# Kernel tuning notes

Hardware: AMD Instinct MI355X
Metric: run time of the kernel (lower is better)

## Reference

```python
import jax, jax.numpy as jnp
import numpy as np

# ---- module config (init kwargs) ----
EMB = 256
HIDDEN = 256
L, H, P = 4, 8, 4
CH = HIDDEN // H
PADDING_MODE = "zeros"   # 'zeros' or 'border'
ALIGN_CORNERS = False
# feature pyramid level shapes (height, width), static
SHAPES = np.array([[128, 128], [64, 64], [32, 32], [16, 16]], dtype=np.int32)
LEVEL_STARTS = np.concatenate([[0], np.cumsum(SHAPES.prod(-1))[:-1]]).astype(np.int32)

B, N = 8, 1024
I = int(SHAPES.prod(-1).sum())  # 21760


def setup_inputs() -> dict:
    key = jax.random.key(0)
    ks = jax.random.split(key, 8)
    scale = 0.02
    return {
        "img": jax.random.normal(ks[0], (B, I, EMB), jnp.float32),
        "img_shapes": jnp.asarray(SHAPES),
        "queries": jax.random.normal(ks[1], (B, N, EMB), jnp.float32),
        "reference_points": jax.random.uniform(ks[2], (B, N, 2), dtype=jnp.float32),
        "W_img": jax.random.normal(ks[3], (EMB, HIDDEN), jnp.float32) * scale,
        "b_img": jnp.zeros((HIDDEN,), jnp.float32),
        "W_q": jax.random.normal(ks[4], (EMB, H * L * P * 3), jnp.float32) * scale,
        "b_q": jnp.zeros((H * L * P * 3,), jnp.float32),
        "W_out": jax.random.normal(ks[5], (HIDDEN, EMB), jnp.float32) * scale,
        "b_out": jnp.zeros((EMB,), jnp.float32),
    }


def _msda(img, points, attn):
    """Multiscale deformable attention core.
    img:    [B, I, H, CH] flattened pyramid features
    points: [B, N, H, L, P, 2] (x, y) in [0, 1]
    attn:   [B, N, H, L, P]
    returns [B, N, H, CH]
    """
    b, _, h_, ch = img.shape
    n = points.shape[1]
    img_t = img.transpose(0, 2, 1, 3)  # [B, H, I, CH]
    levels = []
    for l in range(L):
        hh, ww = int(SHAPES[l, 0]), int(SHAPES[l, 1])
        start = int(LEVEL_STARTS[l])
        p = points[:, :, :, l]  # [B, N, H, P, 2]
        # grid_sample pixel mapping (after the module's 2*p-1 normalization)
        if ALIGN_CORNERS:
            x = p[..., 0] * (ww - 1)
            y = p[..., 1] * (hh - 1)
        else:
            x = p[..., 0] * ww - 0.5
            y = p[..., 1] * hh - 0.5
        x0 = jnp.floor(x); y0 = jnp.floor(y)
        wx = x - x0;       wy = y - y0
        x0i = x0.astype(jnp.int32); y0i = y0.astype(jnp.int32)
        acc = jnp.zeros((b, h_, n * P, ch), img.dtype)
        corners = [
            (x0i,     y0i,     (1 - wx) * (1 - wy)),
            (x0i + 1, y0i,     wx * (1 - wy)),
            (x0i,     y0i + 1, (1 - wx) * wy),
            (x0i + 1, y0i + 1, wx * wy),
        ]
        for xi, yi, cw in corners:
            if PADDING_MODE == "zeros":
                valid = (xi >= 0) & (xi < ww) & (yi >= 0) & (yi < hh)
                cw = cw * valid.astype(cw.dtype)
            xc = jnp.clip(xi, 0, ww - 1)
            yc = jnp.clip(yi, 0, hh - 1)
            idx = start + yc * ww + xc                              # [B, N, H, P]
            idx_t = idx.transpose(0, 2, 1, 3).reshape(b, h_, n * P)  # [B, H, N*P]
            g = jnp.take_along_axis(img_t, idx_t[..., None], axis=2)  # [B, H, N*P, CH]
            cw_t = cw.transpose(0, 2, 1, 3).reshape(b, h_, n * P, 1)
            acc = acc + cw_t * g
        levels.append(acc.reshape(b, h_, n, P, ch))
    samples = jnp.stack(levels, axis=3)            # [B, H, N, L, P, CH]
    attn_t = attn.transpose(0, 2, 1, 3, 4)          # [B, H, N, L, P]
    return jnp.einsum("bhnlpc,bhnlp->bnhc", samples, attn_t)


def reference(img, img_shapes, queries, reference_points, W_img, b_img, W_q, b_q, W_out, b_out):
    b, i_, _ = img.shape
    n = queries.shape[1]
    qp = (queries @ W_q + b_q).reshape(b, n, H, L, P, 3)
    offsets = qp[..., :2]                            # [B, N, H, L, P, 2]
    attn = jax.nn.softmax(qp[..., 2].reshape(b, n, H, L * P), axis=-1).reshape(b, n, H, L, P)
    img_p = (img @ W_img + b_img).reshape(b, i_, H, CH)
    shapes_f = img_shapes.astype(jnp.float32)        # [L, 2] (h, w)
    # faithful to source: offsets / img_shapes[:, None, :]
    sampling_points = reference_points[:, :, None, None, None, :] + offsets / shapes_f[:, None, :]
    out = _msda(img_p, sampling_points, attn)        # [B, N, H, CH]
    return out.reshape(b, n, HIDDEN) @ W_out + b_out
```

## Files before the change

### kernel.cpp

```cpp
#include <hip/hip_runtime.h>
#include <type_traits>
#include <utility>

#define B_    8
#define NQ_   1024
#define I_    21760
#define EMB_  256
#define HID_  256
#define H_    8
#define CH_   32

typedef float  f32x4  __attribute__((ext_vector_type(4)));
typedef __bf16 bf16x8 __attribute__((ext_vector_type(8)));
typedef short  s16x8  __attribute__((ext_vector_type(8)));

template <typename V, typename = void>
struct bf16_mfma_native : std::false_type {};
template <typename V>
struct bf16_mfma_native<V, std::void_t<decltype(__builtin_amdgcn_mfma_f32_16x16x32_bf16(
    std::declval<V>(), std::declval<V>(), std::declval<f32x4>(), 0, 0, 0))>>
    : std::true_type {};

template <typename V>
__device__ __forceinline__ f32x4 mfma_dispatch(V a, V b, f32x4 c) {
  if constexpr (bf16_mfma_native<V>::value) {
    return __builtin_amdgcn_mfma_f32_16x16x32_bf16(a, b, c, 0, 0, 0);
  } else {
    return __builtin_amdgcn_mfma_f32_16x16x32_bf16(
        __builtin_bit_cast(s16x8, a), __builtin_bit_cast(s16x8, b), c, 0, 0, 0);
  }
}

__device__ __forceinline__ f32x4 MFMA(s16x8 a, s16x8 b, f32x4 c) {
  return mfma_dispatch(__builtin_bit_cast(bf16x8, a), __builtin_bit_cast(bf16x8, b), c);
}

__device__ __forceinline__ unsigned short f2bf(float f) {
  unsigned u = __float_as_uint(f);
  u += 0x7fffu + ((u >> 16) & 1u);
  return (unsigned short)(u >> 16);
}

template <int NS, bool OUT_BF16>
__global__ __launch_bounds__(512) void gemm_k256(
    const float* __restrict__ A, const float* __restrict__ W,
    const float* __restrict__ bias, void* __restrict__ Out,
    const int N, const int Mtiles) {
  __shared__ __align__(16) short lds[32 * 264];
  const int tid  = threadIdx.x;
  const int lane = tid & 63;
  const int wave = tid >> 6;
  const int quad = lane >> 4;
  const int ln   = lane & 15;

  s16x8 bfrag[NS][8];
  float bv[NS];
#pragma unroll
  for (int st = 0; st < NS; ++st) {
    const int ng = st * 128 + wave * 16 + ln;
    bv[st] = bias[ng];
#pragma unroll
    for (int ks = 0; ks < 8; ++ks) {
      s16x8 f;
#pragma unroll
      for (int j = 0; j < 8; ++j)
        f[j] = (short)f2bf(W[(ks * 32 + quad * 8 + j) * N + ng]);
      bfrag[st][ks] = f;
    }
  }

  const int sr = tid >> 4;
  const int sc = (tid & 15) * 16;

  for (int t = blockIdx.x; t < Mtiles; t += gridDim.x) {
    const size_t rowBase = (size_t)t * 32;
    {
      const float4* src = (const float4*)(A + (rowBase + sr) * 256 + sc);
      float4 v0 = src[0], v1 = src[1], v2 = src[2], v3 = src[3];
      s16x8 p0, p1;
      p0[0] = (short)f2bf(v0.x); p0[1] = (short)f2bf(v0.y);
      p0[2] = (short)f2bf(v0.z); p0[3] = (short)f2bf(v0.w);
      p0[4] = (short)f2bf(v1.x); p0[5] = (short)f2bf(v1.y);
      p0[6] = (short)f2bf(v1.z); p0[7] = (short)f2bf(v1.w);
      p1[0] = (short)f2bf(v2.x); p1[1] = (short)f2bf(v2.y);
      p1[2] = (short)f2bf(v2.z); p1[3] = (short)f2bf(v2.w);
      p1[4] = (short)f2bf(v3.x); p1[5] = (short)f2bf(v3.y);
      p1[6] = (short)f2bf(v3.z); p1[7] = (short)f2bf(v3.w);
      *(s16x8*)&lds[sr * 264 + sc]     = p0;
      *(s16x8*)&lds[sr * 264 + sc + 8] = p1;
    }
    __syncthreads();

    f32x4 acc[NS][2];
#pragma unroll
    for (int st = 0; st < NS; ++st) {
      acc[st][0] = f32x4{bv[st], bv[st], bv[st], bv[st]};
      acc[st][1] = acc[st][0];
    }
#pragma unroll
    for (int ks = 0; ks < 8; ++ks) {
      s16x8 a0 = *(const s16x8*)&lds[ln * 264 + ks * 32 + quad * 8];
      s16x8 a1 = *(const s16x8*)&lds[(ln + 16) * 264 + ks * 32 + quad * 8];
#pragma unroll
      for (int st = 0; st < NS; ++st) {
        acc[st][0] = MFMA(a0, bfrag[st][ks], acc[st][0]);
        acc[st][1] = MFMA(a1, bfrag[st][ks], acc[st][1]);
      }
    }
#pragma unroll
    for (int st = 0; st < NS; ++st) {
      const int ng = st * 128 + wave * 16 + ln;
#pragma unroll
      for (int rt = 0; rt < 2; ++rt) {
#pragma unroll
        for (int r = 0; r < 4; ++r) {
          const size_t m = rowBase + rt * 16 + quad * 4 + r;
          if constexpr (OUT_BF16)
            ((unsigned short*)Out)[m * N + ng] = f2bf(acc[st][rt][r]);
          else
            ((float*)Out)[m * N + ng] = acc[st][rt][r];
        }
      }
    }
    __syncthreads();
  }
}

__global__ __launch_bounds__(256) void softmax_points_kernel(
    const float* __restrict__ qp, const float* __restrict__ refp,
    float* __restrict__ attn, float* __restrict__ pts) {
  const int gid = blockIdx.x * 256 + threadIdx.x;
  const int q = gid >> 3, h = gid & 7;
  const float* base = qp + (size_t)q * 384 + h * 48;

  float s[16];
  float mx = -1e30f;
#pragma unroll
  for (int lp = 0; lp < 16; ++lp) {
    s[lp] = base[lp * 3 + 2];
    mx = fmaxf(mx, s[lp]);
  }
  float sum = 0.f;
#pragma unroll
  for (int lp = 0; lp < 16; ++lp) {
    s[lp] = __expf(s[lp] - mx);
    sum += s[lp];
  }
  const float inv = 1.0f / sum;
  float* ao = attn + (size_t)gid * 16;
#pragma unroll
  for (int lp = 0; lp < 16; ++lp) ao[lp] = s[lp] * inv;

  const float rx = refp[q * 2], ry = refp[q * 2 + 1];
  float* po = pts + (size_t)gid * 32;
  const float invsh[4] = {1.f / 128.f, 1.f / 64.f, 1.f / 32.f, 1.f / 16.f};
#pragma unroll
  for (int l = 0; l < 4; ++l) {
#pragma unroll
    for (int p = 0; p < 4; ++p) {
      const int lp = l * 4 + p;
      po[lp * 2 + 0] = rx + base[lp * 3 + 0] * invsh[l];
      po[lp * 2 + 1] = ry + base[lp * 3 + 1] * invsh[l];
    }
  }
}

__global__ __launch_bounds__(128) void msda_sample_kernel(
    const unsigned int* __restrict__ imgp,
    const float* __restrict__ attn, const float* __restrict__ pts,
    float* __restrict__ out) {
  __shared__ __align__(16) float sw[128][4];
  __shared__ __align__(16) int   sib[128][4];
  const int bid = blockIdx.x;
  const int b = bid >> 10;
  const int tid = threadIdx.x;

  {
    const int h = tid >> 4, lp = tid & 15, l = lp >> 2;
    const int dims[4]   = {128, 64, 32, 16};
    const int starts[4] = {0, 16384, 20480, 21504};
    const int ww = dims[l], hh = dims[l], start = starts[l];
    const float px = pts[((size_t)bid * 8 + h) * 32 + lp * 2 + 0];
    const float py = pts[((size_t)bid * 8 + h) * 32 + lp * 2 + 1];
    const float a  = attn[((size_t)bid * 8 + h) * 16 + lp];
    const float x = px * (float)ww - 0.5f;
    const float y = py * (float)hh - 0.5f;
    const float x0f = floorf(x), y0f = floorf(y);
    const float wx = x - x0f, wy = y - y0f;
    const int x0 = (int)x0f, y0 = (int)y0f;
    const float cw[4] = {(1.f - wx) * (1.f - wy), wx * (1.f - wy),
                         (1.f - wx) * wy,          wx * wy};
#pragma unroll
    for (int c = 0; c < 4; ++c) {
      const int xi = x0 + (c & 1), yi = y0 + (c >> 1);
      const bool valid = (xi >= 0) & (xi < ww) & (yi >= 0) & (yi < hh);
      const int xc = min(max(xi, 0), ww - 1);
      const int yc = min(max(yi, 0), hh - 1);
      const int idx = start + yc * ww + xc;
      sw[tid][c]  = valid ? a * cw[c] : 0.f;
      sib[tid][c] = ((b * I_ + idx) << 7) + (h << 4);
    }
  }
  __syncthreads();

  const int h = tid >> 4, c2 = tid & 15;
  float acc0 = 0.f, acc1 = 0.f;
#pragma unroll
  for (int lp = 0; lp < 16; ++lp) {
    const float4 w4 = *(const float4*)sw[h * 16 + lp];
    const int4   i4 = *(const int4*)sib[h * 16 + lp];
    unsigned u;
    u = imgp[i4.x + c2];
    acc0 += w4.x * __uint_as_float(u << 16);
    acc1 += w4.x * __uint_as_float(u & 0xffff0000u);
    u = imgp[i4.y + c2];
    acc0 += w4.y * __uint_as_float(u << 16);
    acc1 += w4.y * __uint_as_float(u & 0xffff0000u);
    u = imgp[i4.z + c2];
    acc0 += w4.z * __uint_as_float(u << 16);
    acc1 += w4.z * __uint_as_float(u & 0xffff0000u);
    u = imgp[i4.w + c2];
    acc0 += w4.w * __uint_as_float(u << 16);
    acc1 += w4.w * __uint_as_float(u & 0xffff0000u);
  }
  float2 r;
  r.x = acc0;
  r.y = acc1;
  *(float2*)&out[(size_t)bid * 256 + h * 32 + c2 * 2] = r;
}

#define OFF_IMGP 0ULL
#define OFF_QP   89128960ULL
#define OFF_ATTN 101711872ULL
#define OFF_PTS  105906176ULL
#define OFF_MSDA 114294784ULL
#define WS_NEEDED 122683392ULL

extern "C" void kernel_launch(void* const* d_in, const int* in_sizes, int n_in,
                              void* d_out, int out_size, void* d_ws, size_t ws_size,
                              hipStream_t stream) {
  const float* img     = (const float*)d_in[0];
  const float* queries = (const float*)d_in[2];
  const float* refp    = (const float*)d_in[3];
  const float* W_img   = (const float*)d_in[4];
  const float* b_img   = (const float*)d_in[5];
  const float* W_q     = (const float*)d_in[6];
  const float* b_q     = (const float*)d_in[7];
  const float* W_out   = (const float*)d_in[8];
  const float* b_out   = (const float*)d_in[9];

  if (ws_size < WS_NEEDED) return;

  char* ws = (char*)d_ws;
  unsigned short* imgp = (unsigned short*)(ws + OFF_IMGP);
  float* qp   = (float*)(ws + OFF_QP);
  float* attn = (float*)(ws + OFF_ATTN);
  float* pts  = (float*)(ws + OFF_PTS);
  float* msda = (float*)(ws + OFF_MSDA);

  hipLaunchKernelGGL((gemm_k256<2, true>), dim3(512), dim3(512), 0, stream,
                     img, W_img, b_img, (void*)imgp, 256, I_ * B_ / 32);
  hipLaunchKernelGGL((gemm_k256<3, false>), dim3(256), dim3(512), 0, stream,
                     queries, W_q, b_q, (void*)qp, 384, B_ * NQ_ / 32);
  hipLaunchKernelGGL(softmax_points_kernel, dim3(B_ * NQ_ * H_ / 256), dim3(256), 0, stream,
                     qp, refp, attn, pts);
  hipLaunchKernelGGL(msda_sample_kernel, dim3(B_ * NQ_), dim3(128), 0, stream,
                     (const unsigned int*)imgp, attn, pts, msda);
  hipLaunchKernelGGL((gemm_k256<2, false>), dim3(256), dim3(512), 0, stream,
                     msda, W_out, b_out, d_out, 256, B_ * NQ_ / 32);
}
```

Baseline: 337.8 us.

## Fuse query projection with softmax and widen MSDA sampling per thread

Merges the query projection GEMM and the softmax/sampling-point kernel into one kernel, so the 384-wide projection is staged in shared memory rather than written to and reread from global memory. This removes one launch and the qp buffer. The MSDA sampler now handles 4 queries per 256-thread block, and each thread loads 4 bf16 channels at a time instead of 2. The image projection grid rises from 512 to 544 blocks. The fused kernel reloads the W_q fragments in every one of its 256 blocks and uses one block per 32 rows, so its parallelism may be low.

```diff
diff --git a/kernel.cpp b/kernel.cpp
--- a/kernel.cpp
+++ b/kernel.cpp
@@ -126,65 +126,147 @@
   }
 }
 
-__global__ __launch_bounds__(256) void softmax_points_kernel(
-    const float* __restrict__ qp, const float* __restrict__ refp,
+__global__ __launch_bounds__(512) void qproj_softmax_kernel(
+    const float* __restrict__ A, const float* __restrict__ W,
+    const float* __restrict__ bias, const float* __restrict__ refp,
     float* __restrict__ attn, float* __restrict__ pts) {
-  const int gid = blockIdx.x * 256 + threadIdx.x;
-  const int q = gid >> 3, h = gid & 7;
-  const float* base = qp + (size_t)q * 384 + h * 48;
-
-  float s[16];
-  float mx = -1e30f;
-#pragma unroll
-  for (int lp = 0; lp < 16; ++lp) {
-    s[lp] = base[lp * 3 + 2];
-    mx = fmaxf(mx, s[lp]);
-  }
-  float sum = 0.f;
-#pragma unroll
-  for (int lp = 0; lp < 16; ++lp) {
-    s[lp] = __expf(s[lp] - mx);
-    sum += s[lp];
-  }
-  const float inv = 1.0f / sum;
-  float* ao = attn + (size_t)gid * 16;
-#pragma unroll
-  for (int lp = 0; lp < 16; ++lp) ao[lp] = s[lp] * inv;
-
-  const float rx = refp[q * 2], ry = refp[q * 2 + 1];
-  float* po = pts + (size_t)gid * 32;
-  const float invsh[4] = {1.f / 128.f, 1.f / 64.f, 1.f / 32.f, 1.f / 16.f};
-#pragma unroll
-  for (int l = 0; l < 4; ++l) {
-#pragma unroll
-    for (int p = 0; p < 4; ++p) {
-      const int lp = l * 4 + p;
-      po[lp * 2 + 0] = rx + base[lp * 3 + 0] * invsh[l];
-      po[lp * 2 + 1] = ry + base[lp * 3 + 1] * invsh[l];
-    }
-  }
-}
-
-__global__ __launch_bounds__(128) void msda_sample_kernel(
+  constexpr int N = 384;
+  __shared__ __align__(16) char smem[32 * 392 * 4];
+  short* slds = (short*)smem;
+  float* sout = (float*)smem;
+  const int tid  = threadIdx.x;
+  const int lane = tid & 63;
+  const int wave = tid >> 6;
+  const int quad = lane >> 4;
+  const int ln   = lane & 15;
+
+  s16x8 bfrag[3][8];
+  float bv[3];
+#pragma unroll
+  for (int st = 0; st < 3; ++st) {
+    const int ng = st * 128 + wave * 16 + ln;
+    bv[st] = bias[ng];
+#pragma unroll
+    for (int ks = 0; ks < 8; ++ks) {
+      s16x8 f;
+#pragma unroll
+      for (int j = 0; j < 8; ++j)
+        f[j] = (short)f2bf(W[(ks * 32 + quad * 8 + j) * N + ng]);
+      bfrag[st][ks] = f;
+    }
+  }
+
+  const int sr = tid >> 4;
+  const int sc = (tid & 15) * 16;
+  const size_t rowBase = (size_t)blockIdx.x * 32;
+  {
+    const float4* src = (const float4*)(A + (rowBase + sr) * 256 + sc);
+    float4 v0 = src[0], v1 = src[1], v2 = src[2], v3 = src[3];
+    s16x8 p0, p1;
+    p0[0] = (short)f2bf(v0.x); p0[1] = (short)f2bf(v0.y);
+    p0[2] = (short)f2bf(v0.z); p0[3] = (short)f2bf(v0.w);
+    p0[4] = (short)f2bf(v1.x); p0[5] = (short)f2bf(v1.y);
+    p0[6] = (short)f2bf(v1.z); p0[7] = (short)f2bf(v1.w);
+    p1[0] = (short)f2bf(v2.x); p1[1] = (short)f2bf(v2.y);
+    p1[2] = (short)f2bf(v2.z); p1[3] = (short)f2bf(v2.w);
+    p1[4] = (short)f2bf(v3.x); p1[5] = (short)f2bf(v3.y);
+    p1[6] = (short)f2bf(v3.z); p1[7] = (short)f2bf(v3.w);
+    *(s16x8*)&slds[sr * 264 + sc]     = p0;
+    *(s16x8*)&slds[sr * 264 + sc + 8] = p1;
+  }
+  __syncthreads();
+
+  f32x4 acc[3][2];
+#pragma unroll
+  for (int st = 0; st < 3; ++st) {
+    acc[st][0] = f32x4{bv[st], bv[st], bv[st], bv[st]};
+    acc[st][1] = acc[st][0];
+  }
+#pragma unroll
+  for (int ks = 0; ks < 8; ++ks) {
+    s16x8 a0 = *(const s16x8*)&slds[ln * 264 + ks * 32 + quad * 8];
+    s16x8 a1 = *(const s16x8*)&slds[(ln + 16) * 264 + ks * 32 + quad * 8];
+#pragma unroll
+    for (int st = 0; st < 3; ++st) {
+      acc[st][0] = MFMA(a0, bfrag[st][ks], acc[st][0]);
+      acc[st][1] = MFMA(a1, bfrag[st][ks], acc[st][1]);
+    }
+  }
+  __syncthreads();
+
+#pragma unroll
+  for (int st = 0; st < 3; ++st) {
+    const int ng = st * 128 + wave * 16 + ln;
+#pragma unroll
+    for (int rt = 0; rt < 2; ++rt)
+#pragma unroll
+      for (int r = 0; r < 4; ++r)
+        sout[(rt * 16 + quad * 4 + r) * 392 + ng] = acc[st][rt][r];
+  }
+  __syncthreads();
+
+  if (tid < 256) {
+    const int ql = tid >> 3, h = tid & 7;
+    const float* basep = sout + ql * 392 + h * 48;
+    float s[16];
+    float mx = -1e30f;
+#pragma unroll
+    for (int lp = 0; lp < 16; ++lp) {
+      s[lp] = basep[lp * 3 + 2];
+      mx = fmaxf(mx, s[lp]);
+    }
+    float sum = 0.f;
+#pragma unroll
+    for (int lp = 0; lp < 16; ++lp) {
+      s[lp] = __expf(s[lp] - mx);
+      sum += s[lp];
+    }
+    const float inv = 1.0f / sum;
+    const size_t q   = rowBase + ql;
+    const size_t gq8 = q * 8 + h;
+    float* ao = attn + gq8 * 16;
+#pragma unroll
+    for (int lp = 0; lp < 16; ++lp) ao[lp] = s[lp] * inv;
+
+    const float rx = refp[q * 2], ry = refp[q * 2 + 1];
+    float* po = pts + gq8 * 32;
+    const float invsh[4] = {1.f / 128.f, 1.f / 64.f, 1.f / 32.f, 1.f / 16.f};
+#pragma unroll
+    for (int l = 0; l < 4; ++l) {
+#pragma unroll
+      for (int p = 0; p < 4; ++p) {
+        const int lp = l * 4 + p;
+        po[lp * 2 + 0] = rx + basep[lp * 3 + 0] * invsh[l];
+        po[lp * 2 + 1] = ry + basep[lp * 3 + 1] * invsh[l];
+      }
+    }
+  }
+}
+
+__global__ __launch_bounds__(256) void msda_sample_kernel(
     const unsigned int* __restrict__ imgp,
     const float* __restrict__ attn, const float* __restrict__ pts,
     float* __restrict__ out) {
-  __shared__ __align__(16) float sw[128][4];
-  __shared__ __align__(16) int   sib[128][4];
+  __shared__ __align__(16) float sw[512][4];
+  __shared__ __align__(16) int   sib[512][4];
   const int bid = blockIdx.x;
-  const int b = bid >> 10;
   const int tid = threadIdx.x;
 
-  {
-    const int h = tid >> 4, lp = tid & 15, l = lp >> 2;
-    const int dims[4]   = {128, 64, 32, 16};
-    const int starts[4] = {0, 16384, 20480, 21504};
-    const int ww = dims[l], hh = dims[l], start = starts[l];
-    const float px = pts[((size_t)bid * 8 + h) * 32 + lp * 2 + 0];
-    const float py = pts[((size_t)bid * 8 + h) * 32 + lp * 2 + 1];
-    const float a  = attn[((size_t)bid * 8 + h) * 16 + lp];
-    const float x = px * (float)ww - 0.5f;
-    const float y = py * (float)hh - 0.5f;
+#pragma unroll
+  for (int it = 0; it < 2; ++it) {
+    const int i  = it * 256 + tid;
+    const int q  = i >> 7;
+    const int h  = (i >> 4) & 7;
+    const int lp = i & 15;
+    const int l  = lp >> 2;
+    const int gq = bid * 4 + q;
+    const int b  = gq >> 10;
+    const int ww = 128 >> l;
+    const int start = (l > 0 ? 16384 : 0) + (l > 1 ? 4096 : 0) + (l > 2 ? 1024 : 0);
+    const float2 p = *(const float2*)&pts[((size_t)gq * 8 + h) * 32 + lp * 2];
+    const float a  = attn[((size_t)gq * 8 + h) * 16 + lp];
+    const float x = p.x * (float)ww - 0.5f;
+    const float y = p.y * (float)ww - 0.5f;
     const float x0f = floorf(x), y0f = floorf(y);
     const float wx = x - x0f, wy = y - y0f;
     const int x0 = (int)x0f, y0 = (int)y0f;
@@ -193,48 +275,48 @@
 #pragma unroll
     for (int c = 0; c < 4; ++c) {
       const int xi = x0 + (c & 1), yi = y0 + (c >> 1);
-      const bool valid = (xi >= 0) & (xi < ww) & (yi >= 0) & (yi < hh);
+      const bool valid = (xi >= 0) & (xi < ww) & (yi >= 0) & (yi < ww);
       const int xc = min(max(xi, 0), ww - 1);
-      const int yc = min(max(yi, 0), hh - 1);
+      const int yc = min(max(yi, 0), ww - 1);
       const int idx = start + yc * ww + xc;
-      sw[tid][c]  = valid ? a * cw[c] : 0.f;
-      sib[tid][c] = ((b * I_ + idx) << 7) + (h << 4);
+      sw[i][c]  = valid ? a * cw[c] : 0.f;
+      sib[i][c] = ((b * I_ + idx) << 7) + (h << 4);
     }
   }
   __syncthreads();
 
-  const int h = tid >> 4, c2 = tid & 15;
-  float acc0 = 0.f, acc1 = 0.f;
+  const int q  = tid >> 6;
+  const int h  = (tid >> 3) & 7;
+  const int c4 = tid & 7;
+  float a0 = 0.f, a1 = 0.f, a2 = 0.f, a3 = 0.f;
 #pragma unroll
   for (int lp = 0; lp < 16; ++lp) {
-    const float4 w4 = *(const float4*)sw[h * 16 + lp];
-    const int4   i4 = *(const int4*)sib[h * 16 + lp];
-    unsigned u;
-    u = imgp[i4.x + c2];
-    acc0 += w4.x * __uint_as_float(u << 16);
-    acc1 += w4.x * __uint_as_float(u & 0xffff0000u);
-    u = imgp[i4.y + c2];
-    acc0 += w4.y * __uint_as_float(u << 16);
-    acc1 += w4.y * __uint_as_float(u & 0xffff0000u);
-    u = imgp[i4.z + c2];
-    acc0 += w4.z * __uint_as_float(u << 16);
-    acc1 += w4.z * __uint_as_float(u & 0xffff0000u);
-    u = imgp[i4.w + c2];
-    acc0 += w4.w * __uint_as_float(u << 16);
-    acc1 += w4.w * __uint_as_float(u & 0xffff0000u);
-  }
-  float2 r;
-  r.x = acc0;
-  r.y = acc1;
-  *(float2*)&out[(size_t)bid * 256 + h * 32 + c2 * 2] = r;
+    const int sidx = q * 128 + h * 16 + lp;
+    const float4 w4 = *(const float4*)sw[sidx];
+    const int4   i4 = *(const int4*)sib[sidx];
+    uint2 u;
+#define CORNER(IDX, WGT)                                  \
+    u = *(const uint2*)&imgp[(IDX) + c4 * 2];             \
+    a0 += (WGT) * __uint_as_float(u.x << 16);             \
+    a1 += (WGT) * __uint_as_float(u.x & 0xffff0000u);     \
+    a2 += (WGT) * __uint_as_float(u.y << 16);             \
+    a3 += (WGT) * __uint_as_float(u.y & 0xffff0000u);
+    CORNER(i4.x, w4.x)
+    CORNER(i4.y, w4.y)
+    CORNER(i4.z, w4.z)
+    CORNER(i4.w, w4.w)
+#undef CORNER
+  }
+  const int gq = bid * 4 + q;
+  float4 r{a0, a1, a2, a3};
+  *(float4*)&out[(size_t)gq * 256 + h * 32 + c4 * 4] = r;
 }
 
 #define OFF_IMGP 0ULL
-#define OFF_QP   89128960ULL
-#define OFF_ATTN 101711872ULL
-#define OFF_PTS  105906176ULL
-#define OFF_MSDA 114294784ULL
-#define WS_NEEDED 122683392ULL
+#define OFF_ATTN 89128960ULL
+#define OFF_PTS  93323264ULL
+#define OFF_MSDA 101711872ULL
+#define WS_NEEDED 110100480ULL
 
 extern "C" void kernel_launch(void* const* d_in, const int* in_sizes, int n_in,
                               void* d_out, int out_size, void* d_ws, size_t ws_size,
@@ -253,18 +335,15 @@
 
   char* ws = (char*)d_ws;
   unsigned short* imgp = (unsigned short*)(ws + OFF_IMGP);
-  float* qp   = (float*)(ws + OFF_QP);
   float* attn = (float*)(ws + OFF_ATTN);
   float* pts  = (float*)(ws + OFF_PTS);
   float* msda = (float*)(ws + OFF_MSDA);
 
-  hipLaunchKernelGGL((gemm_k256<2, true>), dim3(512), dim3(512), 0, stream,
+  hipLaunchKernelGGL((gemm_k256<2, true>), dim3(544), dim3(512), 0, stream,
                      img, W_img, b_img, (void*)imgp, 256, I_ * B_ / 32);
-  hipLaunchKernelGGL((gemm_k256<3, false>), dim3(256), dim3(512), 0, stream,
-                     queries, W_q, b_q, (void*)qp, 384, B_ * NQ_ / 32);
-  hipLaunchKernelGGL(softmax_points_kernel, dim3(B_ * NQ_ * H_ / 256), dim3(256), 0, stream,
-                     qp, refp, attn, pts);
-  hipLaunchKernelGGL(msda_sample_kernel, dim3(B_ * NQ_), dim3(128), 0, stream,
+  hipLaunchKernelGGL(qproj_softmax_kernel, dim3(B_ * NQ_ / 32), dim3(512), 0, stream,
+                     queries, W_q, b_q, refp, attn, pts);
+  hipLaunchKernelGGL(msda_sample_kernel, dim3(B_ * NQ_ / 4), dim3(256), 0, stream,
                      (const unsigned int*)imgp, attn, pts, msda);
   hipLaunchKernelGGL((gemm_k256<2, false>), dim3(256), dim3(512), 0, stream,
                      msda, W_out, b_out, d_out, 256, B_ * NQ_ / 32);
```

Result: slower. 359.7 us (+6.5%).
